# Optimization experiments

Hardware: AMD Instinct MI355X
Metric: run time of the kernel (lower is better)

## Reference

```python
import jax, jax.numpy as jnp
import numpy as np

B, T, EMB, H1, H2, NL, LMAX, VOCAB = 32, 20, 32, 64, 128, 4, 1024, 85
EPS = 1e-5

def _lengths():
    # ragged per-structure atom counts, max = 1024 (fixes pad length), sum = 24832
    return 1024 - np.arange(B) * 16

def _lstm(x, Wih0, Whh0, b0, WihS, WhhS, bS):
    """NL-layer batch-first LSTM, torch gate order (i,f,g,o), initial h/c = ones
    (matching the torch code's ones init states). Returns stacked final
    (h, c) per layer, each (NL, batch, hidden)."""
    n = x.shape[0]
    hidden = Whh0.shape[1]
    h_fin, c_fin = [], []
    inp = x
    for l in range(NL):
        Wih = Wih0 if l == 0 else WihS[l - 1]
        Whh = Whh0 if l == 0 else WhhS[l - 1]
        bb = b0 if l == 0 else bS[l - 1]
        xg = jnp.einsum('bti,gi->btg', inp, Wih) + bb  # (n, t, 4*hidden)
        init = (jnp.ones((n, hidden), x.dtype), jnp.ones((n, hidden), x.dtype))
        def step(carry, xt, Whh=Whh):
            h, c = carry
            g = xt + h @ Whh.T
            i, f, gg, o = jnp.split(g, 4, axis=-1)
            c = jax.nn.sigmoid(f) * c + jax.nn.sigmoid(i) * jnp.tanh(gg)
            h = jax.nn.sigmoid(o) * jnp.tanh(c)
            return (h, c), h
        (hT, cT), hs = jax.lax.scan(step, init, jnp.swapaxes(xg, 0, 1))
        inp = jnp.swapaxes(hs, 0, 1)
        h_fin.append(hT)
        c_fin.append(cT)
    return jnp.stack(h_fin), jnp.stack(c_fin)

def _bn_rows(x, g, b):
    # BatchNorm1d(batch_size) applied to x.T in torch: per-row (per-structure)
    # normalization over the feature axis, training-mode (biased var).
    m = x.mean(1, keepdims=True)
    v = x.var(1, keepdims=True)
    return (x - m) * jax.lax.rsqrt(v + EPS) * g[:, None] + b[:, None]

def setup_inputs():
    lengths = _lengths()
    N = int(lengths.sum())
    ks = jax.random.split(jax.random.key(0), 32)
    ki = iter(range(32))
    def nrm(shape, s):
        return s * jax.random.normal(ks[next(ki)], shape, jnp.float32)
    return {
        'neighbor_atom_batch': jax.random.randint(ks[next(ki)], (N * T,), 0, VOCAB, dtype=jnp.int32),
        'neighbors_distan_batch': jax.random.normal(ks[next(ki)], (N * T,), jnp.float32),
        'structure_num_bacth': jnp.asarray(lengths, jnp.int32),
        'batch_idx': jnp.asarray(np.repeat(np.arange(B), lengths), jnp.int32),
        'pos_idx': jnp.asarray(np.concatenate([np.arange(l) for l in lengths]), jnp.int32),
        'embed_w': nrm((VOCAB, EMB), 0.02),
        'l1_Wih0': nrm((4 * H1, EMB), 0.05), 'l1_Whh0': nrm((4 * H1, H1), 0.05), 'l1_b0': nrm((4 * H1,), 0.02),
        'l1_Wih': nrm((NL - 1, 4 * H1, H1), 0.05), 'l1_Whh': nrm((NL - 1, 4 * H1, H1), 0.05), 'l1_b': nrm((NL - 1, 4 * H1), 0.02),
        'l2_Wih0': nrm((4 * H2, H1), 0.05), 'l2_Whh0': nrm((4 * H2, H2), 0.05), 'l2_b0': nrm((4 * H2,), 0.02),
        'l2_Wih': nrm((NL - 1, 4 * H2, H2), 0.05), 'l2_Whh': nrm((NL - 1, 4 * H2, H2), 0.05), 'l2_b': nrm((NL - 1, 4 * H2), 0.02),
        'bn2_g': jnp.ones((B,), jnp.float32), 'bn2_b': jnp.zeros((B,), jnp.float32),
        'bn3_g': jnp.ones((B,), jnp.float32), 'bn3_b': jnp.zeros((B,), jnp.float32),
        'w1': nrm((128, 128), 0.1), 'b1': 0.1 * jnp.ones((128,), jnp.float32),
        'w2': nrm((64, 128), 0.1), 'b2': 0.1 * jnp.ones((64,), jnp.float32),
        'w22': nrm((64, 64), 0.1), 'b22': 0.1 * jnp.ones((64,), jnp.float32),
        'w3': nrm((32, 64), 0.1), 'b3': 0.1 * jnp.ones((32,), jnp.float32),
        'w4': nrm((32, 32), 0.1), 'b4': 0.1 * jnp.ones((32,), jnp.float32),
        'w5': nrm((16, 32), 0.1), 'b5': 0.1 * jnp.ones((16,), jnp.float32),
    }

def reference(neighbor_atom_batch, neighbors_distan_batch, structure_num_bacth,
              batch_idx, pos_idx, embed_w,
              l1_Wih0, l1_Whh0, l1_b0, l1_Wih, l1_Whh, l1_b,
              l2_Wih0, l2_Whh0, l2_b0, l2_Wih, l2_Whh, l2_b,
              bn2_g, bn2_b, bn3_g, bn3_b,
              w1, b1, w2, b2, w22, b22, w3, b3, w4, b4, w5, b5):
    # NOTE: neighbors_distan_batch is an argument of the torch forward but is
    # never used by its body; we keep it for signature fidelity.
    # embed, then scale each embedding row by its own integer atom id (as torch does)
    x = embed_w[neighbor_atom_batch] * neighbor_atom_batch.astype(jnp.float32)[:, None]
    x = x.reshape(-1, T, EMB)                       # (N, 20, 32)
    hT, cT = _lstm(x, l1_Wih0, l1_Whh0, l1_b0, l1_Wih, l1_Whh, l1_b)
    d = hT.mean(0) + cT.mean(0)                     # (N, 64)
    # ragged split by structure_num_bacth + pad_sequence -> (B, LMAX, 64), zero padded
    padded = jnp.zeros((B, LMAX, H1), d.dtype).at[batch_idx, pos_idx].set(d)
    # BatchNorm1d(batch_size): channel dim is the structure index -> stats over (len, feat)
    m = padded.mean((1, 2), keepdims=True)
    v = padded.var((1, 2), keepdims=True)
    padded = (padded - m) * jax.lax.rsqrt(v + EPS) * bn2_g[:, None, None] + bn2_b[:, None, None]
    _, cT2 = _lstm(padded, l2_Wih0, l2_Whh0, l2_b0, l2_Wih, l2_Whh, l2_b)
    d = cT2.mean(0)                                 # (B, 128) mean of final cell states
    d = _bn_rows(d, bn3_g, bn3_b)
    d = jax.nn.relu(d @ w1.T + b1)
    d = jax.nn.relu(d @ w2.T + b2)
    d = _bn_rows(d, bn3_g, bn3_b)                   # same BN layer reused, as in torch
    d = jax.nn.relu(d @ w22.T + b22)
    d = jax.nn.relu(d @ w3.T + b3)
    d = jax.nn.relu(d @ w4.T + b4)
    d = d @ w5.T + b5                               # (B, 16)
    return jax.nn.relu(d.sum(1))                    # (B,)
```

## Files before the change

kernel.cpp:

```cpp
#include <hip/hip_runtime.h>


typedef _Float16 f16x8  __attribute__((ext_vector_type(8)));
typedef float    f32x4  __attribute__((ext_vector_type(4)));

#define DEVI static __device__ __forceinline__

constexpr int   T1c   = 20;
constexpr int   EMBc  = 32;
constexpr int   H1c   = 64;
constexpr int   LMAXc = 1024;
constexpr int   VOCABc= 85;
constexpr int   Ntot  = 24832;
constexpr int   NTc   = Ntot * T1c;
constexpr int   R2c   = 32 * LMAXc;
constexpr float EPSc  = 1e-5f;

DEVI float sigm(float x)   { return 1.f / (1.f + __expf(-x)); }
DEVI float tanhf_(float x) { return 1.f - 2.f / (1.f + __expf(2.f * x)); }

DEVI void barrier_lds() {
    asm volatile("s_waitcnt lgkmcnt(0)\n\ts_barrier" ::: "memory");
}
DEVI void drain_vmem() {
    asm volatile("s_waitcnt vmcnt(0)" ::: "memory");
}

__global__ void __launch_bounds__(256)
k_prepw1(const float* __restrict__ Wih0, const float* __restrict__ Whh0,
         const float* __restrict__ WihS, const float* __restrict__ WhhS,
         _Float16* __restrict__ out)
{
    int i = blockIdx.x * 256 + threadIdx.x;
    if (i >= 4 * 256 * 128) return;
    int l = i >> 15, rem = i & 32767, r = rem >> 7, k = rem & 127;
    float v;
    if (l == 0) {
        if (k < 32)      v = Wih0[r * 32 + k];
        else if (k < 64) v = 0.f;
        else             v = Whh0[r * 64 + (k - 64)];
    } else {
        if (k < 64)      v = WihS[((l - 1) * 256 + r) * 64 + k];
        else             v = WhhS[((l - 1) * 256 + r) * 64 + (k - 64)];
    }
    out[i] = (_Float16)v;
}

__global__ void __launch_bounds__(256)
k_prepw2(const float* __restrict__ Wih0, const float* __restrict__ WihS,
         const float* __restrict__ Whh0, const float* __restrict__ WhhS,
         _Float16* __restrict__ wih, _Float16* __restrict__ whh,
         int* __restrict__ flags)
{
    int i = blockIdx.x * 256 + threadIdx.x;
    if (i < 256) flags[i] = 0;
    if (i >= 2 * 4 * 512 * 128) return;
    int half = i >> 18, rem = i & 262143;
    int l = rem >> 16, r = (rem >> 7) & 511, k = rem & 127;
    if (half == 0) {
        float v = (l == 0) ? ((k < 64) ? Wih0[r * 64 + k] : 0.f)
                           : WihS[((l - 1) * 512 + r) * 128 + k];
        wih[rem] = (_Float16)v;
    } else {
        float v = (l == 0) ? Whh0[r * 128 + k]
                           : WhhS[((l - 1) * 512 + r) * 128 + k];
        whh[rem] = (_Float16)v;
    }
}

__global__ void __launch_bounds__(256)
k_scan1all(const int* __restrict__ atoms, const float* __restrict__ ew,
           const _Float16* __restrict__ W16all,
           const float* __restrict__ b0, const float* __restrict__ bS,
           _Float16* __restrict__ seq, float* __restrict__ dacc)
{
    constexpr int SX = 136;
    __shared__ alignas(16) _Float16 xh[32 * SX];
    __shared__ float ewl[VOCABc * EMBc];
    __shared__ int   aidl[32 * T1c];

    const int tid  = threadIdx.x;
    const int lane = tid & 63;
    const int wv   = tid >> 6;
    const int l16  = lane & 15;
    const int quad = lane >> 4;
    const int n0   = blockIdx.x * 32;
    const int d    = wv * 16 + l16;

    for (int i = tid; i < VOCABc * EMBc; i += 256) ewl[i] = ew[i];
    for (int i = tid; i < 32 * T1c; i += 256) aidl[i] = atoms[n0 * T1c + i];

    float daccv[2][4];
#pragma unroll
    for (int mt = 0; mt < 2; ++mt)
#pragma unroll
        for (int r = 0; r < 4; ++r) daccv[mt][r] = 0.f;

    __syncthreads();

#pragma unroll 1
    for (int l = 0; l < 4; ++l) {
        const _Float16* W16  = W16all + (size_t)l * 256 * 128;
        const float*    bptr = (l == 0) ? b0 : bS + (l - 1) * 256;

        float bias[4];
#pragma unroll
        for (int g = 0; g < 4; ++g) bias[g] = bptr[g * 64 + d];

        f16x8 wF[4][4];
#pragma unroll
        for (int kc = 0; kc < 4; ++kc) {
            const int kb = kc * 32 + quad * 8;
#pragma unroll
            for (int g = 0; g < 4; ++g)
                wF[kc][g] = *(const f16x8*)&W16[(size_t)(g * 64 + d) * 128 + kb];
        }

        f32x4 c[2];
        c[0] = {1.f, 1.f, 1.f, 1.f};
        c[1] = {1.f, 1.f, 1.f, 1.f};

        drain_vmem();
        __syncthreads();

#pragma unroll
        for (int mt = 0; mt < 2; ++mt)
#pragma unroll
            for (int r = 0; r < 4; ++r)
                xh[(mt * 16 + quad * 4 + r) * SX + 64 + d] = (_Float16)1.0f;
        if (l == 0)
            for (int idx = tid; idx < 32 * 32; idx += 256) {
                int s = idx >> 5, e = idx & 31;
                xh[s * SX + 32 + e] = (_Float16)0.f;
            }

#pragma unroll 1
        for (int t = 0; t < T1c; ++t) {
            if (l == 0) {
                for (int idx = tid; idx < 32 * 32; idx += 256) {
                    int s = idx >> 5, e = idx & 31;
                    int id = aidl[s * T1c + t];
                    xh[s * SX + e] = (_Float16)(ewl[id * EMBc + e] * (float)id);
                }
            } else {
                for (int idx = tid; idx < 32 * 8; idx += 256) {
                    int s = idx >> 3, k8 = idx & 7;
                    *(f16x8*)&xh[s * SX + k8 * 8] =
                        *(const f16x8*)&seq[((size_t)(n0 + s) * T1c + t) * H1c + k8 * 8];
                }
            }
            __syncthreads();

            f32x4 acc[2][4];
#pragma unroll
            for (int mt = 0; mt < 2; ++mt)
#pragma unroll
                for (int g = 0; g < 4; ++g)
                    acc[mt][g] = {bias[g], bias[g], bias[g], bias[g]};

#pragma unroll
            for (int kc = 0; kc < 4; ++kc) {
                const int kb = kc * 32 + quad * 8;
                f16x8 ah[2];
#pragma unroll
                for (int mt = 0; mt < 2; ++mt)
                    ah[mt] = *(const f16x8*)&xh[(mt * 16 + l16) * SX + kb];
#pragma unroll
                for (int g = 0; g < 4; ++g)
#pragma unroll
                    for (int mt = 0; mt < 2; ++mt)
                        acc[mt][g] = __builtin_amdgcn_mfma_f32_16x16x32_f16(ah[mt], wF[kc][g], acc[mt][g], 0, 0, 0);
            }
            __syncthreads();

#pragma unroll
            for (int mt = 0; mt < 2; ++mt)
#pragma unroll
                for (int r = 0; r < 4; ++r) {
                    float iv = sigm(acc[mt][0][r]);
                    float fv = sigm(acc[mt][1][r]);
                    float gv = tanhf_(acc[mt][2][r]);
                    float ov = sigm(acc[mt][3][r]);
                    float cv = fv * c[mt][r] + iv * gv;
                    c[mt][r] = cv;
                    float hv = ov * tanhf_(cv);
                    _Float16 hf = (_Float16)hv;
                    int s = mt * 16 + quad * 4 + r;
                    xh[s * SX + 64 + d] = hf;
                    if (l < 3)
                        seq[((size_t)(n0 + s) * T1c + t) * H1c + d] = hf;
                    if (t == T1c - 1)
                        daccv[mt][r] += 0.25f * (hv + cv);
                }
        }
    }
#pragma unroll
    for (int mt = 0; mt < 2; ++mt)
#pragma unroll
        for (int r = 0; r < 4; ++r) {
            int s = mt * 16 + quad * 4 + r;
            dacc[(size_t)(n0 + s) * H1c + d] = daccv[mt][r];
        }
}

__global__ void __launch_bounds__(256)
k_bn2_stats(const int* __restrict__ lens, const float* __restrict__ dacc,
            float* __restrict__ stats)
{
    int b = blockIdx.x;
    int off = 0;
    for (int i = 0; i < b; ++i) off += lens[i];
    int len = lens[b];
    const float* base = dacc + (long)off * H1c;
    float s = 0.f, ss = 0.f;
    int total = len * H1c;
    for (int i = threadIdx.x; i < total; i += 256) { float v = base[i]; s += v; ss += v * v; }
    __shared__ float rs[256], rss[256];
    rs[threadIdx.x] = s; rss[threadIdx.x] = ss;
    __syncthreads();
    for (int st = 128; st > 0; st >>= 1) {
        if (threadIdx.x < st) { rs[threadIdx.x] += rs[threadIdx.x + st]; rss[threadIdx.x] += rss[threadIdx.x + st]; }
        __syncthreads();
    }
    if (threadIdx.x == 0) {
        float m = rs[0] / (float)(LMAXc * H1c);
        float v = rss[0] / (float)(LMAXc * H1c) - m * m;
        stats[b]      = m;
        stats[32 + b] = rsqrtf(fmaxf(v, 0.f) + EPSc);
        stats[64 + b] = (float)off;
    }
}

__global__ void __launch_bounds__(256)
k_bn2_apply(const float* __restrict__ dacc, const float* __restrict__ stats,
            const int* __restrict__ lens, const float* __restrict__ g,
            const float* __restrict__ bb, _Float16* __restrict__ outA)
{
    int i = blockIdx.x * 256 + threadIdx.x;
    if (i >= R2c * 128) return;
    int rr = i >> 7, k = i & 127;
    int b = rr >> 10, p = rr & 1023;
    float y = 0.f;
    if (k < H1c) {
        int off = (int)stats[64 + b];
        float x = (p < lens[b]) ? dacc[(off + p) * H1c + k] : 0.f;
        y = (x - stats[b]) * stats[32 + b] * g[b] + bb[b];
    }
    outA[(size_t)(p * 32 + b) * 128 + k] = (_Float16)y;
}

DEVI float qsel(f32x4 a, int quad) {
    float t01 = (quad & 1) ? a[1] : a[0];
    float t23 = (quad & 1) ? a[3] : a[2];
    return (quad & 2) ? t23 : t01;
}

DEVI void spin_ge(const int* fl, int lane, int need)
{
    for (;;) {
        int f = 0x7fffffff;
        if (lane < 8)
            asm volatile("global_load_dword %0, %1, off sc0 sc1\n\ts_waitcnt vmcnt(0)"
                         : "+v"(f) : "v"(fl) : "memory");
        if (__all(f >= need)) break;
    }
}

__global__ void __launch_bounds__(512, 2)
k_scan2p(const _Float16* __restrict__ seqA,
         const _Float16* __restrict__ wihAll,
         const _Float16* __restrict__ whhAll,
         const float* __restrict__ b0,
         const float* __restrict__ bS,
         _Float16* __restrict__ hbuf,
         int* __restrict__ flags,
         float* __restrict__ c2)
{
    constexpr int SH = 144;
    __shared__ alignas(16) _Float16 av[2][4 * SH];
    __shared__ alignas(16) _Float16 xp[2][4 * SH];

    const int bx   = blockIdx.x;
    const int l    = bx & 3;
    const int g    = bx >> 2;
    const int tid  = threadIdx.x;
    const int lane = tid & 63;
    const int w    = tid >> 6;
    const int l16  = lane & 15;
    const int quad = lane >> 4;
    const int cell = w * 16 + l16;

    const _Float16* Wih = wihAll + (size_t)l * 512 * 128;
    const _Float16* Whh = whhAll + (size_t)l * 512 * 128;
    const float*   bptr = (l == 0) ? b0 : bS + (l - 1) * 512;

    f16x8 wI[4][4], wH[4][4];
    float bia[4];
#pragma unroll
    for (int g4 = 0; g4 < 4; ++g4) {
        bia[g4] = bptr[g4 * 128 + cell];
#pragma unroll
        for (int kc = 0; kc < 4; ++kc) {
            wI[g4][kc] = *(const f16x8*)&Wih[(size_t)(g4 * 128 + cell) * 128 + kc * 32 + quad * 8];
            wH[g4][kc] = *(const f16x8*)&Whh[(size_t)(g4 * 128 + cell) * 128 + kc * 32 + quad * 8];
        }
    }

    const int ci   = tid & 255;
    const int csam = ci >> 6;
    const int coff = ci & 63;

    const int lm = (l > 0) ? (l - 1) : 0;
    const int lp = (l < 3) ? l : 0;

    const unsigned* xdw;
    int xstep;
    if (l == 0) {
        xdw   = (const unsigned*)seqA + ((size_t)(g * 4 + csam)) * 64 + coff;
        xstep = 32 * 64;
    } else {
        xdw   = (const unsigned*)(hbuf + ((size_t)(lm * 8 + g)) * (LMAXc * 512)) + ci;
        xstep = 256;
    }

    _Float16*  hp     = hbuf + ((size_t)(lp * 8 + g)) * (LMAXc * 512) + quad * 128 + cell;
    int*       myflag = flags + (lp * 8 + g) * 8 + w;
    const int* sflag  = flags + (lm * 8 + g) * 8 + (lane & 7);

    { int s = tid >> 7, e = tid & 127; av[0][s * SH + e] = (_Float16)1.0f; }
    float cst = 1.f;

    unsigned rL;
    if (l > 0) spin_ge(sflag, lane, 1);
    {
        unsigned r0;
        if (l == 0)
            asm volatile("global_load_dword %0, %1, off" : "=v"(r0) : "v"(xdw) : "memory");
        else
            asm volatile("global_load_dword %0, %1, off sc0 sc1" : "=v"(r0) : "v"(xdw) : "memory");
        asm volatile("s_waitcnt vmcnt(0)" ::: "memory");
        *(unsigned*)&xp[0][csam * SH + 2 * coff] = r0;
    }
    if (l > 0) spin_ge(sflag, lane, 2);
    {
        const unsigned* p1 = xdw + xstep;
        if (l == 0)
            asm volatile("global_load_dword %0, %1, off" : "=v"(rL) : "v"(p1) : "memory");
        else
            asm volatile("global_load_dword %0, %1, off sc0 sc1" : "=v"(rL) : "v"(p1) : "memory");
    }
    const unsigned* xq = xdw + 2 * (size_t)xstep;
    int fpre = 0;
    __syncthreads();

    int p = 0;
#pragma unroll 1
    for (int t = 0; t < LMAXc; ++t) {
        const _Float16* avR = av[p];
        _Float16*       avW = av[p ^ 1];
        const _Float16* xpR = xp[t & 1];
        _Float16*       xpW = xp[(t + 1) & 1];

        f16x8 ah[4], ax[4];
#pragma unroll
        for (int kc = 0; kc < 4; ++kc) {
            ah[kc] = *(const f16x8*)&avR[(l16 & 3) * SH + kc * 32 + quad * 8];
            ax[kc] = *(const f16x8*)&xpR[(l16 & 3) * SH + kc * 32 + quad * 8];
        }

        f32x4 acc[4];
#pragma unroll
        for (int g4 = 0; g4 < 4; ++g4) acc[g4] = {bia[g4], bia[g4], bia[g4], bia[g4]};
#pragma unroll
        for (int kc = 0; kc < 4; ++kc)
#pragma unroll
            for (int g4 = 0; g4 < 4; ++g4)
                acc[g4] = __builtin_amdgcn_mfma_f32_16x16x32_f16(ax[kc], wI[g4][kc], acc[g4], 0, 0, 0);
#pragma unroll
        for (int kc = 0; kc < 4; ++kc)
#pragma unroll
            for (int g4 = 0; g4 < 4; ++g4)
                acc[g4] = __builtin_amdgcn_mfma_f32_16x16x32_f16(ah[kc], wH[g4][kc], acc[g4], 0, 0, 0);

        asm volatile("s_waitcnt vmcnt(0)" ::: "memory");
        __builtin_amdgcn_sched_barrier(0);
        if (l < 3) {
            if (lane == 0)
                asm volatile("global_store_dword %0, %1, off sc0 sc1"
                             :: "v"(myflag), "v"(t) : "memory");
        }
        if (t < LMAXc - 1)
            *(unsigned*)&xpW[csam * SH + 2 * coff] = rL;

        float gi = qsel(acc[0], quad);
        float gf = qsel(acc[1], quad);
        float gg = qsel(acc[2], quad);
        float go = qsel(acc[3], quad);
        float cv = sigm(gf) * cst + sigm(gi) * tanhf_(gg);
        cst = cv;
        float hv = sigm(go) * tanhf_(cv);
        _Float16 hf = (_Float16)hv;
        avW[quad * SH + cell] = hf;

        if (l > 0 && t <= LMAXc - 3) {
            int need = t + 3;
            if (!__all((lane >= 8) || (fpre >= need))) spin_ge(sflag, lane, need);
        }
        if (t <= LMAXc - 3) {
            if (l == 0)
                asm volatile("global_load_dword %0, %1, off" : "=v"(rL) : "v"(xq) : "memory");
            else
                asm volatile("global_load_dword %0, %1, off sc0 sc1" : "=v"(rL) : "v"(xq) : "memory");
        }
        xq += xstep;
        if (l < 3) {
            unsigned hb = (unsigned)__builtin_bit_cast(unsigned short, hf);
            asm volatile("global_store_short %0, %1, off sc0 sc1"
                         :: "v"(hp), "v"(hb) : "memory");
        }
        hp += 512;
        if (l > 0) {
            if (lane < 8)
                asm volatile("global_load_dword %0, %1, off sc0 sc1"
                             : "+v"(fpre) : "v"(sflag) : "memory");
        }

        barrier_lds();
        p ^= 1;
    }

    asm volatile("s_waitcnt vmcnt(0)" ::: "memory");
    if (l < 3 && lane == 0) {
        int fin = LMAXc;
        asm volatile("global_store_dword %0, %1, off sc0 sc1"
                     :: "v"(myflag), "v"(fin) : "memory");
    }
    c2[(size_t)l * 4096 + (g * 4 + quad) * 128 + cell] = 0.25f * cst;
}

DEVI void bn_rows_dev(float* X, int K, const float* g, const float* bb,
                      float* mv, int tid)
{
    __syncthreads();
    if (tid < 32) {
        float s = 0.f, ss = 0.f;
        const float* r = X + tid * K;
        for (int k = 0; k < K; ++k) { float v = r[k]; s += v; ss += v * v; }
        float m = s / (float)K;
        float vv = ss / (float)K - m * m;
        mv[tid]      = m;
        mv[32 + tid] = rsqrtf(fmaxf(vv, 0.f) + EPSc);
    }
    __syncthreads();
    for (int i = tid; i < 32 * K; i += 256) {
        int b = i / K;
        X[i] = (X[i] - mv[b]) * mv[32 + b] * g[b] + bb[b];
    }
    __syncthreads();
}

DEVI void lin_dev(const float* X, int K, const float* W, const float* bias,
                  int NO, float* Y, int relu, int tid)
{
    __syncthreads();
    for (int i = tid; i < 32 * NO; i += 256) {
        int b = i / NO, j = i - b * NO;
        float a = bias[j];
        const float* xr = X + b * K;
        const float* wr = W + j * K;
        for (int k = 0; k < K; ++k) a += xr[k] * wr[k];
        Y[i] = relu ? fmaxf(a, 0.f) : a;
    }
    __syncthreads();
}

__global__ void __launch_bounds__(256)
k_head(const float* __restrict__ c2, const float* __restrict__ g3, const float* __restrict__ bb3,
       const float* w1, const float* b1, const float* w2, const float* b2,
       const float* w22, const float* b22, const float* w3, const float* b3,
       const float* w4, const float* b4, const float* w5, const float* b5,
       float* __restrict__ out)
{
    __shared__ float A[32 * 128];
    __shared__ float Bf[32 * 128];
    __shared__ float mv[64];
    const int tid = threadIdx.x;

    for (int i = tid; i < 32 * 128; i += 256)
        A[i] = c2[i] + c2[4096 + i] + c2[8192 + i] + c2[12288 + i];
    bn_rows_dev(A, 128, g3, bb3, mv, tid);
    lin_dev(A, 128, w1, b1, 128, Bf, 1, tid);
    lin_dev(Bf, 128, w2, b2, 64, A, 1, tid);
    bn_rows_dev(A, 64, g3, bb3, mv, tid);
    lin_dev(A, 64, w22, b22, 64, Bf, 1, tid);
    lin_dev(Bf, 64, w3, b3, 32, A, 1, tid);
    lin_dev(A, 32, w4, b4, 32, Bf, 1, tid);
    lin_dev(Bf, 32, w5, b5, 16, A, 0, tid);
    if (tid < 32) {
        float s = 0.f;
        for (int j = 0; j < 16; ++j) s += A[tid * 16 + j];
        out[tid] = fmaxf(s, 0.f);
    }
}

extern "C" void kernel_launch(void* const* d_in, const int* in_sizes, int n_in,
                              void* d_out, int out_size, void* d_ws, size_t ws_size,
                              hipStream_t stream)
{
    const int*   atoms  = (const int*)d_in[0];
    const int*   lens   = (const int*)d_in[2];
    const float* embw   = (const float*)d_in[5];
    const float* l1Wih0 = (const float*)d_in[6];
    const float* l1Whh0 = (const float*)d_in[7];
    const float* l1b0   = (const float*)d_in[8];
    const float* l1Wih  = (const float*)d_in[9];
    const float* l1Whh  = (const float*)d_in[10];
    const float* l1b    = (const float*)d_in[11];
    const float* l2Wih0 = (const float*)d_in[12];
    const float* l2Whh0 = (const float*)d_in[13];
    const float* l2b0   = (const float*)d_in[14];
    const float* l2Wih  = (const float*)d_in[15];
    const float* l2Whh  = (const float*)d_in[16];
    const float* l2b    = (const float*)d_in[17];
    const float* bn2g   = (const float*)d_in[18];
    const float* bn2b   = (const float*)d_in[19];
    const float* bn3g   = (const float*)d_in[20];
    const float* bn3b   = (const float*)d_in[21];
    const float* w1  = (const float*)d_in[22]; const float* b1  = (const float*)d_in[23];
    const float* w2  = (const float*)d_in[24]; const float* b2  = (const float*)d_in[25];
    const float* w22 = (const float*)d_in[26]; const float* b22 = (const float*)d_in[27];
    const float* w3  = (const float*)d_in[28]; const float* b3  = (const float*)d_in[29];
    const float* w4  = (const float*)d_in[30]; const float* b4  = (const float*)d_in[31];
    const float* w5  = (const float*)d_in[32]; const float* b5  = (const float*)d_in[33];
    float* out = (float*)d_out;

    char* base = (char*)d_ws;
    size_t off = 0;
    auto take = [&](size_t bytes) -> char* {
        char* p = base + off;
        off = (off + bytes + 255) & ~(size_t)255;
        return p;
    };
    _Float16* seq1f  = (_Float16*)take((size_t)NTc * H1c * 2);
    float*    dacc   = (float*)take((size_t)Ntot * H1c * 4);
    _Float16* wcomb1 = (_Float16*)take((size_t)4 * 256 * 128 * 2);
    _Float16* wih16  = (_Float16*)take((size_t)4 * 512 * 128 * 2);
    _Float16* whh16  = (_Float16*)take((size_t)4 * 512 * 128 * 2);
    _Float16* seqA   = (_Float16*)take((size_t)R2c * 128 * 2);
    _Float16* hbuf   = (_Float16*)take((size_t)3 * 8 * LMAXc * 512 * 2);
    int*      flags  = (int*)take(256 * sizeof(int));
    float*    stats  = (float*)take(1024);
    float*    c2     = (float*)take((size_t)4 * 32 * 128 * 4);

    k_prepw1<<<(4 * 256 * 128 + 255) / 256, 256, 0, stream>>>(l1Wih0, l1Whh0, l1Wih, l1Whh, wcomb1);
    k_prepw2<<<(2 * 4 * 512 * 128 + 255) / 256, 256, 0, stream>>>(l2Wih0, l2Wih, l2Whh0, l2Whh, wih16, whh16, flags);

    k_scan1all<<<Ntot / 32, 256, 0, stream>>>(atoms, embw, wcomb1, l1b0, l1b, seq1f, dacc);

    k_bn2_stats<<<32, 256, 0, stream>>>(lens, dacc, stats);
    k_bn2_apply<<<(R2c * 128 + 255) / 256, 256, 0, stream>>>(dacc, stats, lens, bn2g, bn2b, seqA);

    k_scan2p<<<32, 512, 0, stream>>>(seqA, wih16, whh16, l2b0, l2b, hbuf, flags, c2);

    k_head<<<1, 256, 0, stream>>>(c2, bn3g, bn3b, w1, b1, w2, b2, w22, b22,
                                  w3, b3, w4, b4, w5, b5, out);

    (void)in_sizes; (void)n_in; (void)out_size; (void)ws_size;
}
```

Baseline: 1.816 ms.

## Deepen scan2 prefetch pipeline, unroll by two, split X/H accumulators

Restructures the layer-2 pipelined LSTM scan. The time loop is unrolled by two with fixed buffer parity, and input prefetch goes from one step ahead to two, with a partial vmcnt wait in place of a full drain. Separate X and H accumulators let the input-projection MFMAs run independently of the recurrent chain. Branches on layer index are removed by giving layer 0 a dummy always-ready flag and the last layer its own hbuf slice, at the cost of extra stores and memory, and with a tighter cross-layer handshake.

```diff
diff --git a/kernel.cpp b/kernel.cpp
--- a/kernel.cpp
+++ b/kernel.cpp
@@ -53,7 +53,7 @@
          int* __restrict__ flags)
 {
     int i = blockIdx.x * 256 + threadIdx.x;
-    if (i < 256) flags[i] = 0;
+    if (i < 512) flags[i] = (i < 256) ? 0 : 0x7fffffff;
     if (i >= 2 * 4 * 512 * 128) return;
     int half = i >> 18, rem = i & 262143;
     int l = rem >> 16, r = (rem >> 7) & 511, k = rem & 127;
@@ -266,6 +266,59 @@
     }
 }
 
+#define STEP(T, PAR, R, F)                                                          \
+  {                                                                                 \
+    f32x4 accX[4], accH[4];                                                         \
+    _Pragma("unroll") for (int g4 = 0; g4 < 4; ++g4) {                              \
+        accX[g4] = {bia[g4], bia[g4], bia[g4], bia[g4]};                            \
+        accH[g4] = {0.f, 0.f, 0.f, 0.f};                                            \
+    }                                                                               \
+    _Pragma("unroll") for (int kc = 0; kc < 4; ++kc) {                              \
+        f16x8 ax = *(const f16x8*)&xp[PAR][(l16 & 3) * SH + kc * 32 + quad * 8];    \
+        _Pragma("unroll") for (int g4 = 0; g4 < 4; ++g4)                            \
+            accX[g4] = __builtin_amdgcn_mfma_f32_16x16x32_f16(ax, wI[g4][kc], accX[g4], 0, 0, 0); \
+    }                                                                               \
+    _Pragma("unroll") for (int kc = 0; kc < 4; ++kc) {                              \
+        f16x8 ah = *(const f16x8*)&av[PAR][(l16 & 3) * SH + kc * 32 + quad * 8];    \
+        _Pragma("unroll") for (int g4 = 0; g4 < 4; ++g4)                            \
+            accH[g4] = __builtin_amdgcn_mfma_f32_16x16x32_f16(ah, wH[g4][kc], accH[g4], 0, 0, 0); \
+    }                                                                               \
+    asm volatile("s_waitcnt vmcnt(4)" ::: "memory");                                \
+    __builtin_amdgcn_sched_barrier(0);                                              \
+    if (lane == 0) {                                                                \
+        int fv = (T) - 1;                                                           \
+        asm volatile("global_store_dword %0, %1, off sc0 sc1"                       \
+                     :: "v"(myflag), "v"(fv) : "memory");                           \
+    }                                                                               \
+    *(unsigned*)&xp[PAR ^ 1][csam * SH + 2 * coff] = R;                             \
+    float gi = qsel(accX[0], quad) + qsel(accH[0], quad);                           \
+    float gf = qsel(accX[1], quad) + qsel(accH[1], quad);                           \
+    float gg = qsel(accX[2], quad) + qsel(accH[2], quad);                           \
+    float go = qsel(accX[3], quad) + qsel(accH[3], quad);                           \
+    float cv = sigm(gf) * cst + sigm(gi) * tanhf_(gg);                              \
+    cst = cv;                                                                       \
+    float hv = sigm(go) * tanhf_(cv);                                               \
+    _Float16 hf = (_Float16)hv;                                                     \
+    av[PAR ^ 1][quad * SH + cell] = hf;                                             \
+    {                                                                               \
+        int need = ((T) <= LMAXc - 4) ? (T) + 4 : 0;                                \
+        if (!__all(lane >= 8 || F >= need)) spin_ge(sflag, lane, need);             \
+    }                                                                               \
+    if (l == 0)                                                                     \
+        asm volatile("global_load_dword %0, %1, off" : "=v"(R) : "v"(xq) : "memory"); \
+    else                                                                            \
+        asm volatile("global_load_dword %0, %1, off sc0 sc1" : "=v"(R) : "v"(xq) : "memory"); \
+    if ((T) < LMAXc - 4) xq += xstep;                                               \
+    {   unsigned hb = (unsigned)__builtin_bit_cast(unsigned short, hf);             \
+        asm volatile("global_store_short %0, %1, off sc0 sc1"                       \
+                     :: "v"(hp), "v"(hb) : "memory"); }                             \
+    hp += 512;                                                                      \
+    if (lane < 8)                                                                   \
+        asm volatile("global_load_dword %0, %1, off sc0 sc1"                        \
+                     : "+v"(F) : "v"(sflag) : "memory");                            \
+    barrier_lds();                                                                  \
+  }
+
 __global__ void __launch_bounds__(512, 2)
 k_scan2p(const _Float16* __restrict__ seqA,
          const _Float16* __restrict__ wihAll,
@@ -298,139 +351,81 @@
     float bia[4];
 #pragma unroll
     for (int g4 = 0; g4 < 4; ++g4) {
-        bia[g4] = bptr[g4 * 128 + cell];
 #pragma unroll
         for (int kc = 0; kc < 4; ++kc) {
-            wI[g4][kc] = *(const f16x8*)&Wih[(size_t)(g4 * 128 + cell) * 128 + kc * 32 + quad * 8];
-            wH[g4][kc] = *(const f16x8*)&Whh[(size_t)(g4 * 128 + cell) * 128 + kc * 32 + quad * 8];
+            const _Float16* pI = &Wih[(size_t)(g4 * 128 + cell) * 128 + kc * 32 + quad * 8];
+            const _Float16* pH = &Whh[(size_t)(g4 * 128 + cell) * 128 + kc * 32 + quad * 8];
+            asm volatile("global_load_dwordx4 %0, %1, off" : "=v"(wI[g4][kc]) : "v"(pI));
+            asm volatile("global_load_dwordx4 %0, %1, off" : "=v"(wH[g4][kc]) : "v"(pH));
         }
-    }
+        const float* pb = &bptr[g4 * 128 + cell];
+        asm volatile("global_load_dword %0, %1, off" : "=v"(bia[g4]) : "v"(pb));
+    }
+    drain_vmem();
+    __builtin_amdgcn_sched_barrier(0);
 
     const int ci   = tid & 255;
     const int csam = ci >> 6;
     const int coff = ci & 63;
 
-    const int lm = (l > 0) ? (l - 1) : 0;
-    const int lp = (l < 3) ? l : 0;
-
-    const unsigned* xdw;
+    const unsigned* xq;
     int xstep;
     if (l == 0) {
-        xdw   = (const unsigned*)seqA + ((size_t)(g * 4 + csam)) * 64 + coff;
+        xq    = (const unsigned*)seqA + ((size_t)(g * 4 + csam)) * 64 + coff;
         xstep = 32 * 64;
     } else {
-        xdw   = (const unsigned*)(hbuf + ((size_t)(lm * 8 + g)) * (LMAXc * 512)) + ci;
+        xq    = (const unsigned*)(hbuf + ((size_t)((l - 1) * 8 + g)) * (LMAXc * 512)) + ci;
         xstep = 256;
     }
 
-    _Float16*  hp     = hbuf + ((size_t)(lp * 8 + g)) * (LMAXc * 512) + quad * 128 + cell;
-    int*       myflag = flags + (lp * 8 + g) * 8 + w;
-    const int* sflag  = flags + (lm * 8 + g) * 8 + (lane & 7);
+    _Float16*  hp     = hbuf + ((size_t)(l * 8 + g)) * (LMAXc * 512) + quad * 128 + cell;
+    int*       myflag = flags + (l * 8 + g) * 8 + w;
+    const int* sflag  = (l == 0) ? (flags + 256 + (lane & 7))
+                                 : (flags + ((l - 1) * 8 + g) * 8 + (lane & 7));
 
     { int s = tid >> 7, e = tid & 127; av[0][s * SH + e] = (_Float16)1.0f; }
     float cst = 1.f;
 
-    unsigned rL;
-    if (l > 0) spin_ge(sflag, lane, 1);
+    unsigned rA, rB;
+    int fpreA = 0, fpreB = 0;
+
+    spin_ge(sflag, lane, 1);
+    if (l == 0) asm volatile("global_load_dword %0, %1, off" : "=v"(rA) : "v"(xq) : "memory");
+    else        asm volatile("global_load_dword %0, %1, off sc0 sc1" : "=v"(rA) : "v"(xq) : "memory");
+    drain_vmem();
+    __builtin_amdgcn_sched_barrier(0);
+    *(unsigned*)&xp[0][csam * SH + 2 * coff] = rA;
+
+    spin_ge(sflag, lane, 2);
     {
-        unsigned r0;
-        if (l == 0)
-            asm volatile("global_load_dword %0, %1, off" : "=v"(r0) : "v"(xdw) : "memory");
-        else
-            asm volatile("global_load_dword %0, %1, off sc0 sc1" : "=v"(r0) : "v"(xdw) : "memory");
-        asm volatile("s_waitcnt vmcnt(0)" ::: "memory");
-        *(unsigned*)&xp[0][csam * SH + 2 * coff] = r0;
-    }
-    if (l > 0) spin_ge(sflag, lane, 2);
+        const unsigned* p1 = xq + xstep;
+        if (l == 0) asm volatile("global_load_dword %0, %1, off" : "=v"(rA) : "v"(p1) : "memory");
+        else        asm volatile("global_load_dword %0, %1, off sc0 sc1" : "=v"(rA) : "v"(p1) : "memory");
+    }
+    drain_vmem();
+    __builtin_amdgcn_sched_barrier(0);
+
+    spin_ge(sflag, lane, 3);
     {
-        const unsigned* p1 = xdw + xstep;
-        if (l == 0)
-            asm volatile("global_load_dword %0, %1, off" : "=v"(rL) : "v"(p1) : "memory");
-        else
-            asm volatile("global_load_dword %0, %1, off sc0 sc1" : "=v"(rL) : "v"(p1) : "memory");
-    }
-    const unsigned* xq = xdw + 2 * (size_t)xstep;
-    int fpre = 0;
-    __syncthreads();
-
-    int p = 0;
+        const unsigned* p2 = xq + 2 * xstep;
+        if (l == 0) asm volatile("global_load_dword %0, %1, off" : "=v"(rB) : "v"(p2) : "memory");
+        else        asm volatile("global_load_dword %0, %1, off sc0 sc1" : "=v"(rB) : "v"(p2) : "memory");
+    }
+    if (lane < 8) {
+        asm volatile("global_load_dword %0, %1, off sc0 sc1" : "+v"(fpreA) : "v"(sflag) : "memory");
+        asm volatile("global_load_dword %0, %1, off sc0 sc1" : "+v"(fpreB) : "v"(sflag) : "memory");
+    }
+    xq += 3 * (size_t)xstep;
+    __syncthreads();
+
 #pragma unroll 1
-    for (int t = 0; t < LMAXc; ++t) {
-        const _Float16* avR = av[p];
-        _Float16*       avW = av[p ^ 1];
-        const _Float16* xpR = xp[t & 1];
-        _Float16*       xpW = xp[(t + 1) & 1];
-
-        f16x8 ah[4], ax[4];
-#pragma unroll
-        for (int kc = 0; kc < 4; ++kc) {
-            ah[kc] = *(const f16x8*)&avR[(l16 & 3) * SH + kc * 32 + quad * 8];
-            ax[kc] = *(const f16x8*)&xpR[(l16 & 3) * SH + kc * 32 + quad * 8];
-        }
-
-        f32x4 acc[4];
-#pragma unroll
-        for (int g4 = 0; g4 < 4; ++g4) acc[g4] = {bia[g4], bia[g4], bia[g4], bia[g4]};
-#pragma unroll
-        for (int kc = 0; kc < 4; ++kc)
-#pragma unroll
-            for (int g4 = 0; g4 < 4; ++g4)
-                acc[g4] = __builtin_amdgcn_mfma_f32_16x16x32_f16(ax[kc], wI[g4][kc], acc[g4], 0, 0, 0);
-#pragma unroll
-        for (int kc = 0; kc < 4; ++kc)
-#pragma unroll
-            for (int g4 = 0; g4 < 4; ++g4)
-                acc[g4] = __builtin_amdgcn_mfma_f32_16x16x32_f16(ah[kc], wH[g4][kc], acc[g4], 0, 0, 0);
-
-        asm volatile("s_waitcnt vmcnt(0)" ::: "memory");
-        __builtin_amdgcn_sched_barrier(0);
-        if (l < 3) {
-            if (lane == 0)
-                asm volatile("global_store_dword %0, %1, off sc0 sc1"
-                             :: "v"(myflag), "v"(t) : "memory");
-        }
-        if (t < LMAXc - 1)
-            *(unsigned*)&xpW[csam * SH + 2 * coff] = rL;
-
-        float gi = qsel(acc[0], quad);
-        float gf = qsel(acc[1], quad);
-        float gg = qsel(acc[2], quad);
-        float go = qsel(acc[3], quad);
-        float cv = sigm(gf) * cst + sigm(gi) * tanhf_(gg);
-        cst = cv;
-        float hv = sigm(go) * tanhf_(cv);
-        _Float16 hf = (_Float16)hv;
-        avW[quad * SH + cell] = hf;
-
-        if (l > 0 && t <= LMAXc - 3) {
-            int need = t + 3;
-            if (!__all((lane >= 8) || (fpre >= need))) spin_ge(sflag, lane, need);
-        }
-        if (t <= LMAXc - 3) {
-            if (l == 0)
-                asm volatile("global_load_dword %0, %1, off" : "=v"(rL) : "v"(xq) : "memory");
-            else
-                asm volatile("global_load_dword %0, %1, off sc0 sc1" : "=v"(rL) : "v"(xq) : "memory");
-        }
-        xq += xstep;
-        if (l < 3) {
-            unsigned hb = (unsigned)__builtin_bit_cast(unsigned short, hf);
-            asm volatile("global_store_short %0, %1, off sc0 sc1"
-                         :: "v"(hp), "v"(hb) : "memory");
-        }
-        hp += 512;
-        if (l > 0) {
-            if (lane < 8)
-                asm volatile("global_load_dword %0, %1, off sc0 sc1"
-                             : "+v"(fpre) : "v"(sflag) : "memory");
-        }
-
-        barrier_lds();
-        p ^= 1;
-    }
-
-    asm volatile("s_waitcnt vmcnt(0)" ::: "memory");
-    if (l < 3 && lane == 0) {
+    for (int t = 0; t < LMAXc; t += 2) {
+        STEP(t,     0, rA, fpreA)
+        STEP(t + 1, 1, rB, fpreB)
+    }
+
+    drain_vmem();
+    if (lane == 0) {
         int fin = LMAXc;
         asm volatile("global_store_dword %0, %1, off sc0 sc1"
                      :: "v"(myflag), "v"(fin) : "memory");
@@ -547,8 +542,8 @@
     _Float16* wih16  = (_Float16*)take((size_t)4 * 512 * 128 * 2);
     _Float16* whh16  = (_Float16*)take((size_t)4 * 512 * 128 * 2);
     _Float16* seqA   = (_Float16*)take((size_t)R2c * 128 * 2);
-    _Float16* hbuf   = (_Float16*)take((size_t)3 * 8 * LMAXc * 512 * 2);
-    int*      flags  = (int*)take(256 * sizeof(int));
+    _Float16* hbuf   = (_Float16*)take((size_t)4 * 8 * LMAXc * 512 * 2);
+    int*      flags  = (int*)take(512 * sizeof(int));
     float*    stats  = (float*)take(1024);
     float*    c2     = (float*)take((size_t)4 * 32 * 128 * 4);
 
```

After: 1.739 ms. 1.04x faster.
